# Performance work log

Hardware: AMD Instinct MI355X
Metric: run time of the kernel (lower is better)

## Reference

```python
import jax, jax.numpy as jnp
import numpy as np

P, D, NF, NR, ND, EF, ER = 512, 128, 50000, 50000, 100000, 400000, 400000
BASELINE = 6.0


def setup_inputs() -> dict:
    key = jax.random.key(0)
    ctr = [0]
    def nk():
        ctr[0] += 1
        return jax.random.fold_in(key, ctr[0])
    def nrm(shape, scale=1.0):
        return jax.random.normal(nk(), shape, dtype=jnp.float32) * scale
    def uni(shape):
        return jax.random.uniform(nk(), shape, dtype=jnp.float32)
    def lin(fi, fo):
        return nrm((fi, fo), fi ** -0.5), jnp.zeros((fo,), jnp.float32)
    inp = {}
    inp['target_features'] = nrm((P,))
    inp['form_features'] = nrm((NF, P))
    inp['role_features'] = nrm((NR, P))
    inp['form_binds_y'] = BASELINE + nrm((EF,))
    inp['form_binds_w'] = uni((EF,))
    inp['role_binds_y'] = BASELINE + nrm((ER,))
    inp['role_binds_w'] = uni((ER,))
    inp['form_diff_w'] = uni((NF,)) + 0.01
    inp['role_diff_w'] = uni((NR,)) + 0.01
    inp['trust_vector'] = uni((3,))
    inp['drug_features'] = nrm((ND, D))
    inp['form_w1'], inp['form_b1'] = lin(P, P); inp['form_a1'] = jnp.full((1,), 0.25, jnp.float32)
    inp['form_w2'], inp['form_b2'] = lin(P, P)
    inp['role_w1'], inp['role_b1'] = lin(P, P); inp['role_a1'] = jnp.full((1,), 0.25, jnp.float32)
    inp['role_w2'], inp['role_b2'] = lin(P, P)
    inp['q_w'], inp['q_b'] = lin(P, D)
    inp['k_w'], inp['k_b'] = lin(D, D)
    inp['v_w'], inp['v_b'] = lin(D, D)
    inp['layer_emb'] = nrm((2, 16))
    inp['attn_w1'], inp['attn_b1'] = lin(2 * P + 16, 128)
    inp['attn_w2'], inp['attn_b2'] = lin(128, 64)
    inp['attn_w3'], inp['attn_b3'] = lin(64, 1)
    inp['mix_w1'], inp['mix_b1'] = lin(2 * D + 3, 64); inp['mix_a'] = jnp.full((1,), 0.25, jnp.float32)
    inp['mix_w2'], inp['mix_b2'] = lin(64, 2)
    inp['int_w1'], inp['int_b1'] = lin(D, P); inp['int_a'] = jnp.full((1,), 0.25, jnp.float32)
    inp['int_w2'], inp['int_b2'] = lin(P, P)
    inp['norm_w'] = jnp.ones((P,), jnp.float32)
    inp['norm_b'] = jnp.zeros((P,), jnp.float32)
    inp['delta_gate'] = jnp.float32(0.5)
    inp['form_neighbors'] = jnp.arange(NF, dtype=jnp.int32)
    inp['role_neighbors'] = jnp.arange(NR, dtype=jnp.int32)
    inp['form_binds_src'] = jax.random.randint(nk(), (EF,), 0, NF, dtype=jnp.int32)
    inp['form_binds_dst'] = jax.random.randint(nk(), (EF,), 0, ND, dtype=jnp.int32)
    inp['role_binds_src'] = jax.random.randint(nk(), (ER,), 0, NR, dtype=jnp.int32)
    inp['role_binds_dst'] = jax.random.randint(nk(), (ER,), 0, ND, dtype=jnp.int32)
    return inp


def _prelu(x, a):
    return jnp.where(x >= 0, x, a * x)


def _mlp2(x, w1, b1, a, w2, b2):
    return _prelu(x @ w1 + b1, a) @ w2 + b2


def _ln(x, w=None, b=None, eps=1e-5):
    m = jnp.mean(x, -1, keepdims=True)
    v = jnp.mean((x - m) ** 2, -1, keepdims=True)
    y = (x - m) * jax.lax.rsqrt(v + eps)
    return y if w is None else y * w + b


def _pref(z, nid, src, dst, y, w, drugs, q_w, q_b, k_w, k_b, v_w, v_b):
    # segment-softmax attention over (neighbor protein -> drug) bipartite edges
    N = nid.shape[0]
    order = jnp.argsort(nid)
    s = nid[order]
    pos = jnp.searchsorted(s, src)
    clip = jnp.minimum(pos, N - 1)
    valid = (pos < N) & (s[clip] == src)
    seg = jnp.where(valid, order[clip], N)  # invalid edges -> dump segment N
    q = z @ q_w + q_b                       # [D]
    d = drugs[dst]                          # [E, D] gather
    k = d @ k_w + k_b
    v = (d @ v_w + v_b) * ((y - BASELINE) * w)[:, None]
    logits = (k @ q) / (k.shape[-1] ** 0.5)
    mx = jax.ops.segment_max(logits, seg, num_segments=N + 1)
    mx = jnp.where(jnp.isfinite(mx), mx, 0.0)
    ex = jnp.where(valid, jnp.exp(logits - mx[seg]), 0.0)
    den = jax.ops.segment_sum(ex, seg, num_segments=N + 1) + 1e-12
    attn = ex / den[seg]
    return jax.ops.segment_sum(v * attn[:, None], seg, num_segments=N + 1)[:N]


def _attn_logits(z, zn, lemb, w1, b1, w2, b2, w3, b3):
    N = zn.shape[0]
    x = jnp.concatenate([jnp.broadcast_to(z, (N, z.shape[0])), zn,
                         jnp.broadcast_to(lemb, (N, lemb.shape[0]))], axis=-1)
    h = jax.nn.leaky_relu(x @ w1 + b1, 0.2)
    h = jax.nn.leaky_relu(h @ w2 + b2, 0.2)
    return (h @ w3 + b3)[:, 0]


def _core(fl, form_neighbors, role_neighbors, form_binds_src, form_binds_dst, role_binds_src, role_binds_dst):
    (target_features, form_features, role_features, form_binds_y, form_binds_w,
     role_binds_y, role_binds_w, form_diff_w, role_diff_w, trust_vector, drug_features,
     form_w1, form_b1, form_a1, form_w2, form_b2,
     role_w1, role_b1, role_a1, role_w2, role_b2,
     q_w, q_b, k_w, k_b, v_w, v_b, layer_emb,
     attn_w1, attn_b1, attn_w2, attn_b2, attn_w3, attn_b3,
     mix_w1, mix_b1, mix_a, mix_w2, mix_b2,
     int_w1, int_b1, int_a, int_w2, int_b2,
     norm_w, norm_b, delta_gate) = fl
    z_form = _mlp2(target_features, form_w1, form_b1, form_a1, form_w2, form_b2)
    z_role = _mlp2(target_features, role_w1, role_b1, role_a1, role_w2, role_b2)
    z = 0.5 * (z_form + z_role)
    form_feats = _mlp2(form_features, form_w1, form_b1, form_a1, form_w2, form_b2)
    role_feats = _mlp2(role_features, role_w1, role_b1, role_a1, role_w2, role_b2)
    form_msgs = _pref(z, form_neighbors, form_binds_src, form_binds_dst, form_binds_y, form_binds_w, drug_features, q_w, q_b, k_w, k_b, v_w, v_b)
    role_msgs = _pref(z, role_neighbors, role_binds_src, role_binds_dst, role_binds_y, role_binds_w, drug_features, q_w, q_b, k_w, k_b, v_w, v_b)
    form_logits = _attn_logits(z, form_feats, layer_emb[0], attn_w1, attn_b1, attn_w2, attn_b2, attn_w3, attn_b3)
    role_logits = _attn_logits(z, role_feats, layer_emb[1], attn_w1, attn_b1, attn_w2, attn_b2, attn_w3, attn_b3)
    form_attn = jax.nn.softmax(form_logits + jnp.log(jnp.maximum(form_diff_w, 1e-12)))
    role_attn = jax.nn.softmax(role_logits + jnp.log(jnp.maximum(role_diff_w, 1e-12)))
    v_form = form_attn @ form_msgs
    v_role = role_attn @ role_msgs
    mixer_in = jnp.concatenate([v_form, v_role, trust_vector])
    lw = jax.nn.softmax(_mlp2(mixer_in, mix_w1, mix_b1, mix_a, mix_w2, mix_b2))
    w_form, w_role = lw[0], lw[1]
    v_prior = w_form * v_form + w_role * v_role
    form_delta = form_attn @ (z[None, :] - form_feats)
    role_delta = role_attn @ (z[None, :] - role_feats)
    delta_raw = w_form * form_delta + w_role * role_delta
    delta_mean = delta_gate * _ln(delta_raw)
    z_refined = _ln(z + _mlp2(v_prior, int_w1, int_b1, int_a, int_w2, int_b2), norm_w, norm_b)
    return z_refined, v_prior, delta_mean


def reference(target_features, form_features, role_features, form_binds_y, form_binds_w, role_binds_y, role_binds_w, form_diff_w, role_diff_w, trust_vector, drug_features, form_w1, form_b1, form_a1, form_w2, form_b2, role_w1, role_b1, role_a1, role_w2, role_b2, q_w, q_b, k_w, k_b, v_w, v_b, layer_emb, attn_w1, attn_b1, attn_w2, attn_b2, attn_w3, attn_b3, mix_w1, mix_b1, mix_a, mix_w2, mix_b2, int_w1, int_b1, int_a, int_w2, int_b2, norm_w, norm_b, delta_gate, form_neighbors, role_neighbors, form_binds_src, form_binds_dst, role_binds_src, role_binds_dst):
    fl = (target_features, form_features, role_features, form_binds_y, form_binds_w,
          role_binds_y, role_binds_w, form_diff_w, role_diff_w, trust_vector, drug_features,
          form_w1, form_b1, form_a1, form_w2, form_b2,
          role_w1, role_b1, role_a1, role_w2, role_b2,
          q_w, q_b, k_w, k_b, v_w, v_b, layer_emb,
          attn_w1, attn_b1, attn_w2, attn_b2, attn_w3, attn_b3,
          mix_w1, mix_b1, mix_a, mix_w2, mix_b2,
          int_w1, int_b1, int_a, int_w2, int_b2,
          norm_w, norm_b, delta_gate)
    return _core(fl, form_neighbors, role_neighbors, form_binds_src, form_binds_dst, role_binds_src, role_binds_dst)
```

## Files before the change

kernel.cpp:

```cpp
#include <hip/hip_runtime.h>

#define NFN 50000
#define NDR 100000
#define NE  400000
#define MT  391
#define M0PAD 50048

__device__ __forceinline__ float bf2f(unsigned short u) {
    return __uint_as_float(((unsigned)u) << 16);
}
__device__ __forceinline__ unsigned short f2bf(float f) {
    unsigned u = __float_as_uint(f);
    unsigned r = 0x7FFFu + ((u >> 16) & 1u);
    return (unsigned short)((u + r) >> 16);
}

typedef __attribute__((ext_vector_type(8))) short bf16x8;
typedef __attribute__((ext_vector_type(4))) float f32x4;

struct KArgs {
    const float *tf, *ff, *rf, *fby, *fbw, *rby, *rbw, *fdw, *rdw, *trust, *drugs;
    const float *fw1, *fb1, *fa1, *fw2, *fb2, *rw1, *rb1, *ra1, *rw2, *rb2;
    const float *qw, *qb, *kw, *kb, *vw, *vb, *lemb;
    const float *aw1, *ab1, *aw2, *ab2, *aw3, *ab3;
    const float *mw1, *mb1, *ma, *mw2, *mb2;
    const float *iw1, *ib1, *ia, *iw2, *ib2;
    const float *nw, *nb, *dgate;
    const int *fsrc, *fdst, *rsrc, *rdst;
    float *shf, *shr;
    float *svf, *svr;
    float *gdenf, *gdenr;
    float *edenf, *edenr;
    float *cdf, *cdr;
    float *hraw;
    float *zraw;
    float *qraw;
    float *b1f, *b1r;
    float *sfr;
    float *o2raw;
    float *qk, *c0, *pe;
    unsigned short *w1tf, *w1tr;
    unsigned short *w2atf, *w2atr;
    unsigned short *aw2t;
    float *nexf, *nexr;
    unsigned short *H;
    unsigned short *Xb;
    float *hi;
    float *wfwr;
    float *out;
};

__global__ __launch_bounds__(512) void kA(KArgs A) {
    const int b = blockIdx.x;
    const int side = b >> 5, chunk = b & 31;
    const int tt = threadIdx.x;
    const float* w1 = side ? A.rw1 : A.fw1;
    float acc = 0.f;
    const int i0 = chunk * 16;
#pragma unroll
    for (int k = 0; k < 16; k++) {
        int i = i0 + k;
        acc = fmaf(A.tf[i], w1[(size_t)i * 512 + tt], acc);
    }
    atomicAdd(&A.hraw[side * 512 + tt], acc);
}

__global__ __launch_bounds__(512) void kB(KArgs A) {
    const int b = blockIdx.x;
    const int side = b >> 4, chunk = b & 15;
    const int tt = threadIdx.x;
    const float* w2 = side ? A.rw2 : A.fw2;
    const float* b1 = side ? A.rb1 : A.fb1;
    const float aa = (side ? A.ra1 : A.fa1)[0];
    float acc = 0.f;
    const int i0 = chunk * 32;
    for (int k = 0; k < 32; k++) {
        int i = i0 + k;
        float h = A.hraw[side * 512 + i] + b1[i];
        h = h >= 0.f ? h : aa * h;
        acc = fmaf(h, w2[(size_t)i * 512 + tt], acc);
    }
    if (b == 0) acc += A.fb2[tt] + A.rb2[tt];
    atomicAdd(&A.zraw[tt], acc);
}

__global__ __launch_bounds__(512) void kC1(KArgs A) {
    const int b = blockIdx.x;
    const int t = threadIdx.x;
    const int j = t & 127, isub = t >> 7;
    if (b < 8) {
        const int i0 = b * 64 + isub * 16;
        float acc = 0.f;
        for (int k = 0; k < 16; k++) {
            int i = i0 + k;
            acc = fmaf(0.5f * A.zraw[i], A.qw[(size_t)i * 128 + j], acc);
        }
        atomicAdd(&A.qraw[j], acc);
        if (b == 0 && t < 128) atomicAdd(&A.qraw[t], A.qb[t]);
    } else if (b < 16) {
        const int chunk = b - 8;
        const int i0 = chunk * 64 + isub * 16;
        float acc = 0.f;
        for (int k = 0; k < 16; k++) {
            int i = i0 + k;
            acc = fmaf(0.5f * A.zraw[i], A.aw1[(size_t)i * 128 + j], acc);
            acc = fmaf(A.fb2[i], A.aw1[(size_t)(512 + i) * 128 + j], acc);
        }
        atomicAdd(&A.b1f[j], acc);
        if (b == 8 && t < 128) {
            float c = A.ab1[t];
            for (int l = 0; l < 16; l++) c = fmaf(A.lemb[l], A.aw1[(size_t)(1024 + l) * 128 + t], c);
            atomicAdd(&A.b1f[t], c);
        }
    } else {
        const int chunk = b - 16;
        const int i0 = chunk * 64 + isub * 16;
        float acc = 0.f;
        for (int k = 0; k < 16; k++) {
            int i = i0 + k;
            acc = fmaf(0.5f * A.zraw[i], A.aw1[(size_t)i * 128 + j], acc);
            acc = fmaf(A.rb2[i], A.aw1[(size_t)(512 + i) * 128 + j], acc);
        }
        atomicAdd(&A.b1r[j], acc);
        if (b == 16 && t < 128) {
            float c = A.ab1[t];
            for (int l = 0; l < 16; l++) c = fmaf(A.lemb[16 + l], A.aw1[(size_t)(1024 + l) * 128 + t], c);
            atomicAdd(&A.b1r[t], c);
        }
    }
}

__global__ __launch_bounds__(256) void kC2(KArgs A) {
    const int t = threadIdx.x;
    __shared__ float sq[128];
    if (t < 128) sq[t] = A.qraw[t];
    __syncthreads();
    if (t < 128) {
        float s = 0.f;
        for (int j = 0; j < 128; j++) s = fmaf(A.kw[t * 128 + j], sq[j], s);
        A.qk[t] = s;
    } else if (t == 128) {
        float c = 0.f;
        for (int j = 0; j < 128; j++) c = fmaf(A.kb[j], sq[j], c);
        A.c0[0] = c;
    }
}

__global__ __launch_bounds__(256) void k_cvtX2(KArgs A) {
    const int XN4 = NFN * 512 / 4;
    const int P4 = M0PAD * 512 / 4;
    int idx = blockIdx.x * 256 + threadIdx.x;
    const int stride = gridDim.x * 256;
    for (; idx < 2 * XN4; idx += stride) {
        const int side = idx >= XN4;
        const int li = idx - side * XN4;
        float4 v = ((const float4*)(side ? A.rf : A.ff))[li];
        uint2 o;
        o.x = (unsigned)f2bf(v.x) | ((unsigned)f2bf(v.y) << 16);
        o.y = (unsigned)f2bf(v.z) | ((unsigned)f2bf(v.w) << 16);
        ((uint2*)A.Xb)[(size_t)side * P4 + li] = o;
    }
}

__global__ __launch_bounds__(512) void k_cvtW(KArgs A) {
    const int side = blockIdx.x >> 9;
    const int k = blockIdx.x & 511;
    const int n = threadIdx.x;
    const float* w1 = side ? A.rw1 : A.fw1;
    unsigned short* o = side ? A.w1tr : A.w1tf;
    o[(size_t)n * 512 + k] = f2bf(w1[k * 512 + n]);
}

__global__ __launch_bounds__(128) void k_cvtA2(KArgs A) {
    const int j = blockIdx.x;
    const int i = threadIdx.x;
    A.aw2t[j * 128 + i] = f2bf(A.aw2[i * 64 + j]);
}

__global__ __launch_bounds__(128) void k_w2a(KArgs A) {
    const int side = blockIdx.x >> 9;
    const int i = blockIdx.x & 511;
    const int j = threadIdx.x;
    const float* w2 = side ? A.rw2 : A.fw2;
    unsigned short* outp = side ? A.w2atr : A.w2atf;
    float s = 0.f;
    for (int k = 0; k < 512; k++)
        s = fmaf(w2[i * 512 + k], A.aw1[(size_t)(512 + k) * 128 + j], s);
    outp[(size_t)j * 512 + i] = f2bf(s);
}

__global__ __launch_bounds__(256, 2)
void mfma_gemm(KArgs A) {
    __shared__ __align__(16) unsigned short Abuf[2][128 * 32];
    __shared__ __align__(16) unsigned short Bbuf[2][128 * 32];
    const int t = threadIdx.x;
    const int lane = t & 63, wv = t >> 6;
    const int p = blockIdx.x;
    const int L = (p & 7) * MT + (p >> 3);
    const int side = L >= (MT * 4);
    const int lbid = L - side * (MT * 4);
    const int m0l = (lbid >> 2) * 128, n0 = (lbid & 3) * 128;
    const unsigned short* __restrict__ Ab = A.Xb + (size_t)side * M0PAD * 512;
    const unsigned short* __restrict__ Bt = side ? A.w1tr : A.w1tf;
    const float* __restrict__ bias = side ? A.rb1 : A.fb1;
    const float aval = (side ? A.ra1 : A.fa1)[0];
    unsigned short* __restrict__ Cv = A.H + (size_t)side * M0PAD * 512;
    const int wm = (wv >> 1) * 64, wn = (wv & 1) * 64;
    const int lm = lane & 15, ko = lane >> 4;
    const int K = 512;

    f32x4 acc[4][4];
#pragma unroll
    for (int i = 0; i < 4; i++)
#pragma unroll
        for (int j = 0; j < 4; j++) acc[i][j] = (f32x4){0.f, 0.f, 0.f, 0.f};

    auto stage = [&](int buf, int k0) {
#pragma unroll
        for (int ii = 0; ii < 2; ii++) {
            const int inst = wv * 2 + ii;
            const int rl = inst * 16 + (lane >> 2);
            const int sl = (lane & 3) ^ ((rl >> 1) & 3);
            int ar = m0l + rl; if (ar >= NFN) ar = NFN - 1;
            __builtin_amdgcn_global_load_lds(
                (const __attribute__((address_space(1))) void*)(Ab + (size_t)ar * K + k0 + sl * 8),
                (__attribute__((address_space(3))) void*)(&Abuf[buf][inst * 512]), 16, 0, 0);
            __builtin_amdgcn_global_load_lds(
                (const __attribute__((address_space(1))) void*)(Bt + (size_t)(n0 + rl) * K + k0 + sl * 8),
                (__attribute__((address_space(3))) void*)(&Bbuf[buf][inst * 512]), 16, 0, 0);
        }
    };

    auto compute = [&](int buf) {
        bf16x8 af[4], bfr[4];
#pragma unroll
        for (int mi = 0; mi < 4; mi++) {
            int row = wm + mi * 16 + lm;
            af[mi] = *(const bf16x8*)&Abuf[buf][row * 32 + ((ko ^ ((row >> 1) & 3)) * 8)];
        }
#pragma unroll
        for (int ni = 0; ni < 4; ni++) {
            int col = wn + ni * 16 + lm;
            bfr[ni] = *(const bf16x8*)&Bbuf[buf][col * 32 + ((ko ^ ((col >> 1) & 3)) * 8)];
        }
#pragma unroll
        for (int mi = 0; mi < 4; mi++)
#pragma unroll
            for (int ni = 0; ni < 4; ni++)
                acc[mi][ni] = __builtin_amdgcn_mfma_f32_16x16x32_bf16(af[mi], bfr[ni], acc[mi][ni], 0, 0, 0);
    };

    stage(0, 0);
    __syncthreads();
    for (int kt = 0; kt < 16; kt++) {
        if (kt + 1 < 16) stage((kt + 1) & 1, (kt + 1) * 32);
        compute(kt & 1);
        __syncthreads();
    }

#pragma unroll
    for (int mi = 0; mi < 4; mi++) {
#pragma unroll
        for (int reg = 0; reg < 4; reg++) {
            int row = m0l + wm + mi * 16 + ko * 4 + reg;
#pragma unroll
            for (int ni = 0; ni < 4; ni++) {
                int col = n0 + wn + ni * 16 + lm;
                float v = acc[mi][ni][reg] + bias[col];
                v = v >= 0.f ? v : aval * v;
                Cv[(size_t)row * 512 + col] = f2bf(v);
            }
        }
    }
}

__global__ __launch_bounds__(256, 2)
void gemm_logits(KArgs A) {
    __shared__ __align__(16) unsigned short Abuf[2][128 * 32];
    __shared__ __align__(16) unsigned short Bbuf[2][128 * 32];
    __shared__ __align__(16) unsigned short Gs[128][136];
    __shared__ float ps[128];
    __shared__ float red2[128];
    const int bid = blockIdx.x;
    const int side = bid >= MT;
    const int m0l = (bid - side * MT) * 128;
    const unsigned short* __restrict__ Ab = A.H + (size_t)side * M0PAD * 512;
    const unsigned short* __restrict__ Bt = side ? A.w2atr : A.w2atf;
    const float* __restrict__ bias = side ? A.b1r : A.b1f;
    const float* __restrict__ dw = side ? A.rdw : A.fdw;
    float* __restrict__ nex = side ? A.nexr : A.nexf;
    float* __restrict__ gden = side ? A.gdenr : A.gdenf;
    const int t = threadIdx.x;
    const int lane = t & 63, wv = t >> 6;
    const int wm = (wv >> 1) * 64, wn = (wv & 1) * 64;
    const int lm = lane & 15, ko = lane >> 4;
    const int K = 512;

    f32x4 acc[4][4];
#pragma unroll
    for (int i = 0; i < 4; i++)
#pragma unroll
        for (int j = 0; j < 4; j++) acc[i][j] = (f32x4){0.f, 0.f, 0.f, 0.f};

    auto stage = [&](int buf, int k0) {
#pragma unroll
        for (int ii = 0; ii < 2; ii++) {
            const int inst = wv * 2 + ii;
            const int rl = inst * 16 + (lane >> 2);
            const int sl = (lane & 3) ^ ((rl >> 1) & 3);
            int ar = m0l + rl; if (ar >= NFN) ar = NFN - 1;
            __builtin_amdgcn_global_load_lds(
                (const __attribute__((address_space(1))) void*)(Ab + (size_t)ar * K + k0 + sl * 8),
                (__attribute__((address_space(3))) void*)(&Abuf[buf][inst * 512]), 16, 0, 0);
            __builtin_amdgcn_global_load_lds(
                (const __attribute__((address_space(1))) void*)(Bt + (size_t)rl * K + k0 + sl * 8),
                (__attribute__((address_space(3))) void*)(&Bbuf[buf][inst * 512]), 16, 0, 0);
        }
    };

    auto compute = [&](int buf) {
        bf16x8 af[4], bfr[4];
#pragma unroll
        for (int mi = 0; mi < 4; mi++) {
            int row = wm + mi * 16 + lm;
            af[mi] = *(const bf16x8*)&Abuf[buf][row * 32 + ((ko ^ ((row >> 1) & 3)) * 8)];
        }
#pragma unroll
        for (int ni = 0; ni < 4; ni++) {
            int col = wn + ni * 16 + lm;
            bfr[ni] = *(const bf16x8*)&Bbuf[buf][col * 32 + ((ko ^ ((col >> 1) & 3)) * 8)];
        }
#pragma unroll
        for (int mi = 0; mi < 4; mi++)
#pragma unroll
            for (int ni = 0; ni < 4; ni++)
                acc[mi][ni] = __builtin_amdgcn_mfma_f32_16x16x32_bf16(af[mi], bfr[ni], acc[mi][ni], 0, 0, 0);
    };

    stage(0, 0);
    __syncthreads();
    for (int kt = 0; kt < 16; kt++) {
        if (kt + 1 < 16) stage((kt + 1) & 1, (kt + 1) * 32);
        compute(kt & 1);
        __syncthreads();
    }

#pragma unroll
    for (int mi = 0; mi < 4; mi++) {
#pragma unroll
        for (int reg = 0; reg < 4; reg++) {
            int row_l = wm + mi * 16 + ko * 4 + reg;
#pragma unroll
            for (int ni = 0; ni < 4; ni++) {
                int col = wn + ni * 16 + lm;
                float v = acc[mi][ni][reg] + bias[col];
                v = v >= 0.f ? v : 0.2f * v;
                Gs[row_l][col] = f2bf(v);
            }
        }
    }
    __syncthreads();

    const int wr0 = wv * 32;
    float ab2v[4], aw3v[4];
#pragma unroll
    for (int ni = 0; ni < 4; ni++) {
        int col = ni * 16 + lm;
        ab2v[ni] = A.ab2[col];
        aw3v[ni] = A.aw3[col];
    }
    f32x4 acc2[2][4];
#pragma unroll
    for (int i = 0; i < 2; i++)
#pragma unroll
        for (int j = 0; j < 4; j++) acc2[i][j] = (f32x4){0.f, 0.f, 0.f, 0.f};
#pragma unroll
    for (int kk = 0; kk < 4; kk++) {
        bf16x8 ga[2], bb[4];
#pragma unroll
        for (int mi = 0; mi < 2; mi++)
            ga[mi] = *(const bf16x8*)&Gs[wr0 + mi * 16 + lm][kk * 32 + ko * 8];
#pragma unroll
        for (int ni = 0; ni < 4; ni++)
            bb[ni] = *(const bf16x8*)(A.aw2t + (size_t)(ni * 16 + lm) * 128 + kk * 32 + ko * 8);
#pragma unroll
        for (int mi = 0; mi < 2; mi++)
#pragma unroll
            for (int ni = 0; ni < 4; ni++)
                acc2[mi][ni] = __builtin_amdgcn_mfma_f32_16x16x32_bf16(ga[mi], bb[ni], acc2[mi][ni], 0, 0, 0);
    }
#pragma unroll
    for (int mi = 0; mi < 2; mi++) {
#pragma unroll
        for (int reg = 0; reg < 4; reg++) {
            float s = 0.f;
#pragma unroll
            for (int ni = 0; ni < 4; ni++) {
                float v = acc2[mi][ni][reg] + ab2v[ni];
                v = v >= 0.f ? v : 0.2f * v;
                s = fmaf(v, aw3v[ni], s);
            }
            s += __shfl_xor(s, 1, 64);
            s += __shfl_xor(s, 2, 64);
            s += __shfl_xor(s, 4, 64);
            s += __shfl_xor(s, 8, 64);
            if (lm == 0) ps[wr0 + mi * 16 + ko * 4 + reg] = s;
        }
    }
    __syncthreads();
    float val = 0.f;
    if (t < 128) {
        int node = m0l + t;
        if (node < NFN) {
            val = expf(ps[t] + A.ab3[0] + logf(fmaxf(dw[node], 1e-12f)));
            nex[node] = val;
        }
        red2[t] = val;
    }
    __syncthreads();
    if (t < 64) red2[t] += red2[t + 64];
    __syncthreads();
    if (t < 32) red2[t] += red2[t + 32];
    __syncthreads();
    if (t < 16) red2[t] += red2[t + 16];
    __syncthreads();
    if (t == 0) {
        float s = 0.f;
        for (int i = 0; i < 16; i++) s += red2[i];
        atomicAdd(gden, s);
    }
}

__global__ __launch_bounds__(256) void k_wsumH(KArgs A) {
    const int side = blockIdx.y;
    const int t = threadIdx.x;
    const int sub = t >> 6, colb = (t & 63) * 8;
    const float* nex = side ? A.nexr : A.nexf;
    const float invden = 1.0f / *(side ? A.gdenr : A.gdenf);
    float* SH = side ? A.shr : A.shf;
    const unsigned short* Hs = A.H + (size_t)side * M0PAD * 512;
    float acc[8];
#pragma unroll
    for (int c = 0; c < 8; c++) acc[c] = 0.f;
    for (int rp = blockIdx.x; rp < NFN / 4; rp += gridDim.x) {
        const int row = rp * 4 + sub;
        const float a = nex[row] * invden;
        uint4 v = *(const uint4*)(Hs + (size_t)row * 512 + colb);
        unsigned vv[4] = {v.x, v.y, v.z, v.w};
#pragma unroll
        for (int u = 0; u < 4; u++) {
            acc[2 * u + 0] = fmaf(a, bf2f((unsigned short)(vv[u] & 0xFFFFu)), acc[2 * u + 0]);
            acc[2 * u + 1] = fmaf(a, bf2f((unsigned short)(vv[u] >> 16)), acc[2 * u + 1]);
        }
    }
    __shared__ float red[4][512];
#pragma unroll
    for (int c = 0; c < 8; c++) red[sub][colb + c] = acc[c];
    __syncthreads();
#pragma unroll
    for (int h = 0; h < 2; h++) {
        const int col = t + h * 256;
        atomicAdd(&SH[col], red[0][col] + red[1][col] + red[2][col] + red[3][col]);
    }
}

__global__ __launch_bounds__(256) void k_pd(KArgs A) {
    const int lane = threadIdx.x & 63;
    const int gw = blockIdx.x * 4 + (threadIdx.x >> 6);
    const int nw = gridDim.x * 4;
    const float2 qk2 = *(const float2*)(A.qk + 2 * lane);
    const float c0 = A.c0[0];
    for (int dr = gw; dr < NDR; dr += nw) {
        float2 dv = *(const float2*)(A.drugs + (size_t)dr * 128 + 2 * lane);
        float p = fmaf(dv.x, qk2.x, dv.y * qk2.y);
        for (int off = 32; off >= 1; off >>= 1) p += __shfl_xor(p, off, 64);
        if (lane == 0) A.pe[dr] = expf((p + c0) * 0.088388347648318447f);
    }
}

__global__ __launch_bounds__(256) void k_edge1(KArgs A) {
    const int side = blockIdx.y;
    const int* src = side ? A.rsrc : A.fsrc;
    const int* dst = side ? A.rdst : A.fdst;
    float* eden = side ? A.edenr : A.edenf;
    const int base = blockIdx.x * 1024 + threadIdx.x;
#pragma unroll
    for (int u = 0; u < 4; u++) {
        const int e = base + u * 256;
        if (e < NE) atomicAdd(&eden[src[e]], A.pe[dst[e]]);
    }
}

__global__ __launch_bounds__(256) void k_nfac(KArgs A) {
    const int side = blockIdx.y;
    const int n = blockIdx.x * 256 + threadIdx.x;
    if (n >= NFN) return;
    const float* nex = side ? A.nexr : A.nexf;
    float* eden = side ? A.edenr : A.edenf;
    const float invden = 1.0f / *(side ? A.gdenr : A.gdenf);
    eden[n] = nex[n] * invden / (eden[n] + 1e-12f);
}

__global__ __launch_bounds__(256) void k_edge2(KArgs A) {
    const int side = blockIdx.y;
    const int* src = side ? A.rsrc : A.fsrc;
    const int* dst = side ? A.rdst : A.fdst;
    const float* yy = side ? A.rby : A.fby;
    const float* ww = side ? A.rbw : A.fbw;
    const float* fac = side ? A.edenr : A.edenf;
    float* cd = side ? A.cdr : A.cdf;
    float* sv = side ? A.svr : A.svf;
    const int base = blockIdx.x * 1024 + threadIdx.x;
    float csum = 0.f;
#pragma unroll
    for (int u = 0; u < 4; u++) {
        const int e = base + u * 256;
        if (e < NE) {
            float coef = fac[src[e]] * A.pe[dst[e]] * ((yy[e] - 6.0f) * ww[e]);
            atomicAdd(&cd[dst[e]], coef);
            csum += coef;
        }
    }
    __shared__ float red[256];
    red[threadIdx.x] = csum; __syncthreads();
    for (int s2 = 128; s2 >= 1; s2 >>= 1) {
        if (threadIdx.x < s2) red[threadIdx.x] += red[threadIdx.x + s2];
        __syncthreads();
    }
    if (threadIdx.x == 0) atomicAdd(&sv[128], red[0]);
}

__global__ __launch_bounds__(256) void k_wsumD(KArgs A) {
    const int t = threadIdx.x;
    const int col = t & 127, rg = t >> 7;
    __shared__ float red[2][2][128];
    float af = 0.f, ar = 0.f;
    for (int dr = blockIdx.x * 2 + rg; dr < NDR; dr += gridDim.x * 2) {
        float cf = A.cdf[dr], cr = A.cdr[dr];
        float dv = A.drugs[(size_t)dr * 128 + col];
        af = fmaf(cf, dv, af);
        ar = fmaf(cr, dv, ar);
    }
    red[rg][0][col] = af; red[rg][1][col] = ar;
    __syncthreads();
    if (rg == 0) {
        atomicAdd(&A.svf[col], red[0][0][col] + red[1][0][col]);
        atomicAdd(&A.svr[col], red[0][1][col] + red[1][1][col]);
    }
}

__global__ __launch_bounds__(512) void kF1(KArgs A) {
    const int b = blockIdx.x;
    const int side = b >> 3, chunk = b & 7;
    const int tt = threadIdx.x;
    const float* w2 = side ? A.rw2 : A.fw2;
    const float* SH = side ? A.shr : A.shf;
    float acc = 0.f;
    const int i0 = chunk * 64;
    for (int k = 0; k < 64; k++) {
        int i = i0 + k;
        acc = fmaf(SH[i], w2[(size_t)i * 512 + tt], acc);
    }
    if (chunk == 0) acc += (side ? A.rb2 : A.fb2)[tt];
    atomicAdd(&A.sfr[side * 512 + tt], acc);
}

__global__ __launch_bounds__(512) void kF2(KArgs A) {
    const int t = threadIdx.x;
    __shared__ float vform[128], vrole[128], vprior[128], mh[64], sw[2];
    if (t < 128) {
        float vf = A.svf[128] * A.vb[t];
        float vr = A.svr[128] * A.vb[t];
        for (int i = 0; i < 128; i++) {
            vf = fmaf(A.svf[i], A.vw[i * 128 + t], vf);
            vr = fmaf(A.svr[i], A.vw[i * 128 + t], vr);
        }
        vform[t] = vf; vrole[t] = vr;
    }
    __syncthreads();
    if (t < 64) {
        float m = A.mb1[t];
        for (int i = 0; i < 128; i++) m = fmaf(vform[i], A.mw1[i * 64 + t], m);
        for (int i = 0; i < 128; i++) m = fmaf(vrole[i], A.mw1[(128 + i) * 64 + t], m);
        for (int i = 0; i < 3; i++)   m = fmaf(A.trust[i], A.mw1[(256 + i) * 64 + t], m);
        float ma = A.ma[0];
        mh[t] = m >= 0.f ? m : ma * m;
    }
    __syncthreads();
    if (t < 2) {
        float o = A.mb2[t];
        for (int i = 0; i < 64; i++) o = fmaf(mh[i], A.mw2[i * 2 + t], o);
        sw[t] = o;
    }
    __syncthreads();
    const float mo = fmaxf(sw[0], sw[1]);
    const float e0 = expf(sw[0] - mo), e1 = expf(sw[1] - mo);
    const float wf = e0 / (e0 + e1), wr = e1 / (e0 + e1);
    if (t == 0) { A.wfwr[0] = wf; A.wfwr[1] = wr; }
    if (t < 128) {
        float vp = wf * vform[t] + wr * vrole[t];
        vprior[t] = vp;
        A.out[512 + t] = vp;
    }
    __syncthreads();
    float hi = A.ib1[t];
    for (int i = 0; i < 128; i++) hi = fmaf(vprior[i], A.iw1[(size_t)i * 512 + t], hi);
    float ia = A.ia[0];
    A.hi[t] = hi >= 0.f ? hi : ia * hi;
}

__global__ __launch_bounds__(512) void kF3(KArgs A) {
    const int chunk = blockIdx.x;
    const int tt = threadIdx.x;
    float acc = 0.f;
    const int i0 = chunk * 64;
    for (int k = 0; k < 64; k++) {
        int i = i0 + k;
        acc = fmaf(A.hi[i], A.iw2[(size_t)i * 512 + tt], acc);
    }
    if (chunk == 0) acc += A.ib2[tt];
    atomicAdd(&A.o2raw[tt], acc);
}

__global__ __launch_bounds__(512) void kF4(KArgs A) {
    const int t = threadIdx.x;
    __shared__ float red[512];
    const float wf = A.wfwr[0], wr = A.wfwr[1];
    const float zv = 0.5f * A.zraw[t];
    float dr_ = zv - wf * A.sfr[t] - wr * A.sfr[512 + t];
    red[t] = dr_; __syncthreads();
    for (int s = 256; s >= 1; s >>= 1) { if (t < s) red[t] += red[t + s]; __syncthreads(); }
    float mean = red[0] * (1.f / 512.f); __syncthreads();
    float dd = dr_ - mean;
    red[t] = dd * dd; __syncthreads();
    for (int s = 256; s >= 1; s >>= 1) { if (t < s) red[t] += red[t + s]; __syncthreads(); }
    float var = red[0] * (1.f / 512.f); __syncthreads();
    A.out[640 + t] = A.dgate[0] * (dd * rsqrtf(var + 1e-5f));
    float zin = zv + A.o2raw[t];
    red[t] = zin; __syncthreads();
    for (int s = 256; s >= 1; s >>= 1) { if (t < s) red[t] += red[t + s]; __syncthreads(); }
    float mean2 = red[0] * (1.f / 512.f); __syncthreads();
    float d2 = zin - mean2;
    red[t] = d2 * d2; __syncthreads();
    for (int s = 256; s >= 1; s >>= 1) { if (t < s) red[t] += red[t + s]; __syncthreads(); }
    float var2 = red[0] * (1.f / 512.f);
    A.out[t] = (d2 * rsqrtf(var2 + 1e-5f)) * A.nw[t] + A.nb[t];
}

extern "C" void kernel_launch(void* const* d_in, const int* in_sizes, int n_in,
                              void* d_out, int out_size, void* d_ws, size_t ws_size,
                              hipStream_t stream) {
    (void)in_sizes; (void)n_in; (void)out_size;
    KArgs A;
    A.tf    = (const float*)d_in[0];
    A.ff    = (const float*)d_in[1];
    A.rf    = (const float*)d_in[2];
    A.fby   = (const float*)d_in[3];
    A.fbw   = (const float*)d_in[4];
    A.rby   = (const float*)d_in[5];
    A.rbw   = (const float*)d_in[6];
    A.fdw   = (const float*)d_in[7];
    A.rdw   = (const float*)d_in[8];
    A.trust = (const float*)d_in[9];
    A.drugs = (const float*)d_in[10];
    A.fw1 = (const float*)d_in[11]; A.fb1 = (const float*)d_in[12]; A.fa1 = (const float*)d_in[13];
    A.fw2 = (const float*)d_in[14]; A.fb2 = (const float*)d_in[15];
    A.rw1 = (const float*)d_in[16]; A.rb1 = (const float*)d_in[17]; A.ra1 = (const float*)d_in[18];
    A.rw2 = (const float*)d_in[19]; A.rb2 = (const float*)d_in[20];
    A.qw = (const float*)d_in[21]; A.qb = (const float*)d_in[22];
    A.kw = (const float*)d_in[23]; A.kb = (const float*)d_in[24];
    A.vw = (const float*)d_in[25]; A.vb = (const float*)d_in[26];
    A.lemb = (const float*)d_in[27];
    A.aw1 = (const float*)d_in[28]; A.ab1 = (const float*)d_in[29];
    A.aw2 = (const float*)d_in[30]; A.ab2 = (const float*)d_in[31];
    A.aw3 = (const float*)d_in[32]; A.ab3 = (const float*)d_in[33];
    A.mw1 = (const float*)d_in[34]; A.mb1 = (const float*)d_in[35]; A.ma = (const float*)d_in[36];
    A.mw2 = (const float*)d_in[37]; A.mb2 = (const float*)d_in[38];
    A.iw1 = (const float*)d_in[39]; A.ib1 = (const float*)d_in[40]; A.ia = (const float*)d_in[41];
    A.iw2 = (const float*)d_in[42]; A.ib2 = (const float*)d_in[43];
    A.nw = (const float*)d_in[44]; A.nb = (const float*)d_in[45];
    A.dgate = (const float*)d_in[46];
    A.fsrc = (const int*)d_in[49];
    A.fdst = (const int*)d_in[50];
    A.rsrc = (const int*)d_in[51];
    A.rdst = (const int*)d_in[52];
    A.out = (float*)d_out;

    char* w = (char*)d_ws;
    size_t off = 0;
    auto alloc = [&](size_t bytes) -> void* {
        void* p = w + off;
        off = (off + bytes + 255) & ~(size_t)255;
        return p;
    };
    A.shf   = (float*)alloc(512 * 4);
    A.shr   = (float*)alloc(512 * 4);
    A.svf   = (float*)alloc(129 * 4);
    A.svr   = (float*)alloc(129 * 4);
    A.gdenf = (float*)alloc(4);
    A.gdenr = (float*)alloc(4);
    A.edenf = (float*)alloc((size_t)NFN * 4);
    A.edenr = (float*)alloc((size_t)NFN * 4);
    A.cdf   = (float*)alloc((size_t)NDR * 4);
    A.cdr   = (float*)alloc((size_t)NDR * 4);
    A.hraw  = (float*)alloc(1024 * 4);
    A.zraw  = (float*)alloc(512 * 4);
    A.qraw  = (float*)alloc(128 * 4);
    A.b1f   = (float*)alloc(128 * 4);
    A.b1r   = (float*)alloc(128 * 4);
    A.sfr   = (float*)alloc(1024 * 4);
    A.o2raw = (float*)alloc(512 * 4);
    const size_t zbytes = off;
    A.qk   = (float*)alloc(128 * 4);
    A.c0   = (float*)alloc(4);
    A.pe   = (float*)alloc((size_t)NDR * 4);
    A.w1tf = (unsigned short*)alloc((size_t)512 * 512 * 2);
    A.w1tr = (unsigned short*)alloc((size_t)512 * 512 * 2);
    A.w2atf = (unsigned short*)alloc((size_t)128 * 512 * 2);
    A.w2atr = (unsigned short*)alloc((size_t)128 * 512 * 2);
    A.aw2t  = (unsigned short*)alloc((size_t)64 * 128 * 2);
    A.nexf  = (float*)alloc((size_t)NFN * 4);
    A.nexr  = (float*)alloc((size_t)NFN * 4);
    A.H     = (unsigned short*)alloc((size_t)2 * M0PAD * 512 * 2);
    A.Xb    = (unsigned short*)alloc((size_t)2 * M0PAD * 512 * 2);
    A.hi    = (float*)alloc(512 * 4);
    A.wfwr  = (float*)alloc(2 * 4);
    if (ws_size && off > ws_size) return;

    hipMemsetAsync(d_ws, 0, zbytes, stream);

    kA<<<64, 512, 0, stream>>>(A);
    kB<<<32, 512, 0, stream>>>(A);
    kC1<<<24, 512, 0, stream>>>(A);
    kC2<<<1, 256, 0, stream>>>(A);
    k_cvtW<<<1024, 512, 0, stream>>>(A);
    k_cvtA2<<<64, 128, 0, stream>>>(A);
    k_w2a<<<1024, 128, 0, stream>>>(A);
    k_pd<<<1024, 256, 0, stream>>>(A);

    const int EB4 = (NE + 1023) / 1024;
    const int NFB = (NFN + 255) / 256;
    k_cvtX2<<<2048, 256, 0, stream>>>(A);
    mfma_gemm<<<2 * MT * 4, 256, 0, stream>>>(A);
    gemm_logits<<<2 * MT, 256, 0, stream>>>(A);
    k_wsumH<<<dim3(1024, 2), 256, 0, stream>>>(A);
    k_edge1<<<dim3(EB4, 2), 256, 0, stream>>>(A);
    k_nfac<<<dim3(NFB, 2), 256, 0, stream>>>(A);
    k_edge2<<<dim3(EB4, 2), 256, 0, stream>>>(A);
    k_wsumD<<<512, 256, 0, stream>>>(A);
    kF1<<<16, 512, 0, stream>>>(A);
    kF2<<<1, 512, 0, stream>>>(A);
    kF3<<<8, 512, 0, stream>>>(A);
    kF4<<<1, 512, 0, stream>>>(A);
}
```

Baseline: 494.7 us.

## Fuse softmax-weighted H row sum into gemm_logits epilogue, defer normalization

Removes the separate k_wsumH kernel. Each gemm_logits block now accumulates the unnormalized exp-weighted sum of its 128 H rows and adds it to SH with atomics. Division by the global denominator moves into kF1, since it is linear and only available after all blocks finish. This saves one launch and a full re-read of H from a separate pass, at the cost of extra per-thread work and 512 atomics per block in the GEMM epilogue.

```diff
diff --git a/kernel.cpp b/kernel.cpp
--- a/kernel.cpp
+++ b/kernel.cpp
@@ -281,6 +281,7 @@
     __shared__ __align__(16) unsigned short Gs[128][136];
     __shared__ float ps[128];
     __shared__ float red2[128];
+    __shared__ float snex[128];
     const int bid = blockIdx.x;
     const int side = bid >= MT;
     const int m0l = (bid - side * MT) * 128;
@@ -415,6 +416,7 @@
             val = expf(ps[t] + A.ab3[0] + logf(fmaxf(dw[node], 1e-12f)));
             nex[node] = val;
         }
+        snex[t] = val;
         red2[t] = val;
     }
     __syncthreads();
@@ -429,38 +431,21 @@
         for (int i = 0; i < 16; i++) s += red2[i];
         atomicAdd(gden, s);
     }
-}
-
-__global__ __launch_bounds__(256) void k_wsumH(KArgs A) {
-    const int side = blockIdx.y;
-    const int t = threadIdx.x;
-    const int sub = t >> 6, colb = (t & 63) * 8;
-    const float* nex = side ? A.nexr : A.nexf;
-    const float invden = 1.0f / *(side ? A.gdenr : A.gdenf);
-    float* SH = side ? A.shr : A.shf;
-    const unsigned short* Hs = A.H + (size_t)side * M0PAD * 512;
-    float acc[8];
-#pragma unroll
-    for (int c = 0; c < 8; c++) acc[c] = 0.f;
-    for (int rp = blockIdx.x; rp < NFN / 4; rp += gridDim.x) {
-        const int row = rp * 4 + sub;
-        const float a = nex[row] * invden;
-        uint4 v = *(const uint4*)(Hs + (size_t)row * 512 + colb);
-        unsigned vv[4] = {v.x, v.y, v.z, v.w};
-#pragma unroll
-        for (int u = 0; u < 4; u++) {
-            acc[2 * u + 0] = fmaf(a, bf2f((unsigned short)(vv[u] & 0xFFFFu)), acc[2 * u + 0]);
-            acc[2 * u + 1] = fmaf(a, bf2f((unsigned short)(vv[u] >> 16)), acc[2 * u + 1]);
-        }
-    }
-    __shared__ float red[4][512];
-#pragma unroll
-    for (int c = 0; c < 8; c++) red[sub][colb + c] = acc[c];
-    __syncthreads();
-#pragma unroll
-    for (int h = 0; h < 2; h++) {
-        const int col = t + h * 256;
-        atomicAdd(&SH[col], red[0][col] + red[1][col] + red[2][col] + red[3][col]);
+    {
+        const unsigned short* Hrow = Ab + (size_t)m0l * 512;
+        float a0 = 0.f, a1 = 0.f;
+        for (int r = 0; r < 128; r += 2) {
+            const float w0 = snex[r], w1 = snex[r + 1];
+            const unsigned v0 = *(const unsigned*)(Hrow + (size_t)r * 512 + 2 * t);
+            const unsigned v1 = *(const unsigned*)(Hrow + (size_t)(r + 1) * 512 + 2 * t);
+            a0 = fmaf(w0, bf2f((unsigned short)(v0 & 0xFFFFu)), a0);
+            a1 = fmaf(w0, bf2f((unsigned short)(v0 >> 16)), a1);
+            a0 = fmaf(w1, bf2f((unsigned short)(v1 & 0xFFFFu)), a0);
+            a1 = fmaf(w1, bf2f((unsigned short)(v1 >> 16)), a1);
+        }
+        float* SH = side ? A.shr : A.shf;
+        atomicAdd(&SH[2 * t], a0);
+        atomicAdd(&SH[2 * t + 1], a1);
     }
 }
 
@@ -555,12 +540,14 @@
     const int tt = threadIdx.x;
     const float* w2 = side ? A.rw2 : A.fw2;
     const float* SH = side ? A.shr : A.shf;
+    const float invden = 1.0f / *(side ? A.gdenr : A.gdenf);
     float acc = 0.f;
     const int i0 = chunk * 64;
     for (int k = 0; k < 64; k++) {
         int i = i0 + k;
         acc = fmaf(SH[i], w2[(size_t)i * 512 + tt], acc);
     }
+    acc *= invden;
     if (chunk == 0) acc += (side ? A.rb2 : A.fb2)[tt];
     atomicAdd(&A.sfr[side * 512 + tt], acc);
 }
@@ -743,7 +730,6 @@
     k_cvtX2<<<2048, 256, 0, stream>>>(A);
     mfma_gemm<<<2 * MT * 4, 256, 0, stream>>>(A);
     gemm_logits<<<2 * MT, 256, 0, stream>>>(A);
-    k_wsumH<<<dim3(1024, 2), 256, 0, stream>>>(A);
     k_edge1<<<dim3(EB4, 2), 256, 0, stream>>>(A);
     k_nfac<<<dim3(NFB, 2), 256, 0, stream>>>(A);
     k_edge2<<<dim3(EB4, 2), 256, 0, stream>>>(A);
```

Measured after the change: 486.1 us. About the same (-1.7%).
